# Kernel optimization log

Hardware: AMD Instinct MI355X
Metric: run time of the kernel (lower is better)

The kernel has to match this reference:

```python
import jax, jax.numpy as jnp
import numpy as np

D = 256      # d_model (module-level constant in source)
H = 4        # num_heads
HD = D // H  # head dim = 64
B = 16
T = 512
STEP = 0.5   # self.step_size
NEG = -1e9
SCALE = 1.0 / np.sqrt(HD).astype(np.float32)


def _ln(x, g, b):
    m = jnp.mean(x, -1, keepdims=True)
    v = jnp.var(x, -1, keepdims=True)
    return (x - m) / jnp.sqrt(v + 1e-5) * g + b


def _forward(x, h0,
             sa_wq, sa_wk, sa_wv, sa_wo, sa_bq, sa_bk, sa_bv, sa_bo,
             f_w1, f_b1, f_w2, f_b2,
             ta_wq, ta_wk, ta_wv, ta_wo, ta_bq, ta_bk, ta_bv, ta_bo,
             tr_w1, tr_b1, tr_w2, tr_b2,
             ps_w, ps_b, sp_w, sp_b,
             ln1_g, ln1_b, ln2_g, ln2_b, ln3_g, ln3_b, ln4_g, ln4_b):
    Bz, Tz, Dz = x.shape
    # ---- causal self-attention over parallel_repr ----
    q = (x @ sa_wq + sa_bq).reshape(Bz, Tz, H, HD)
    k = (x @ sa_wk + sa_bk).reshape(Bz, Tz, H, HD)
    v = (x @ sa_wv + sa_bv).reshape(Bz, Tz, H, HD)
    scores = jnp.einsum('bqhd,bkhd->bhqk', q, k) * SCALE
    causal = jnp.tril(jnp.ones((Tz, Tz), bool))
    scores = jnp.where(causal, scores, NEG)
    attn = jnp.einsum('bhqk,bkhd->bqhd', jax.nn.softmax(scores, -1), v)
    attn = attn.reshape(Bz, Tz, Dz) @ sa_wo + sa_bo
    x = _ln(x + attn, ln1_g, ln1_b)
    # ---- FFN with sequential guidance ----
    guid = h0 @ sp_w + sp_b                      # sequential_to_parallel, [B, D]
    ffn_in = x + 0.3 * guid[:, None, :]
    ffn = jax.nn.gelu(ffn_in @ f_w1 + f_b1, approximate=False) @ f_w2 + f_b2
    x = _ln(x + ffn, ln2_g, ln2_b)
    # ---- sequential scan with growing-cache trajectory attention ----
    # past states only enter through their K/V projections, so project each
    # new state once when it is appended (same math as re-projecting the cache).
    def step(carry, inp):
        h, kbuf, vbuf = carry                    # kbuf/vbuf: [T, B, H, HD]
        t, xt = inp                              # xt: [B, D]
        qt = (xt @ ta_wq + ta_bq).reshape(Bz, H, HD)
        sc = jnp.einsum('bhd,tbhd->bht', qt, kbuf) * SCALE
        valid = (jnp.arange(Tz) < t)[None, None, :]
        ctx = jnp.einsum('bht,tbhd->bhd',
                         jax.nn.softmax(jnp.where(valid, sc, NEG), -1), vbuf)
        ctx = ctx.reshape(Bz, Dz) @ ta_wo + ta_bo
        ctx = jnp.where(t > 0, ctx, 0.0)         # torch code zeroes context at t=0
        pg = xt @ ps_w + ps_b                    # parallel_to_sequential
        comb = jnp.concatenate([xt + 0.3 * pg, ctx], -1)
        delta = jax.nn.gelu(comb @ tr_w1 + tr_b1, approximate=False) @ tr_w2 + tr_b2
        h = _ln(h + STEP * delta, ln3_g, ln3_b)
        kbuf = kbuf.at[t].set((h @ ta_wk + ta_bk).reshape(Bz, H, HD))
        vbuf = vbuf.at[t].set((h @ ta_wv + ta_bv).reshape(Bz, H, HD))
        return (h, kbuf, vbuf), None

    buf0 = jnp.zeros((Tz, Bz, H, HD), x.dtype)
    (hT, _, _), _ = jax.lax.scan(step, (h0, buf0, buf0),
                                 (jnp.arange(Tz), jnp.swapaxes(x, 0, 1)))
    return x, _ln(hT, ln4_g, ln4_b)


def setup_inputs() -> dict:
    ks = iter(jax.random.split(jax.random.key(0), 64))
    def w(*shape):
        return jax.random.normal(next(ks), shape, jnp.float32) * 0.02
    inp = {
        'x': jax.random.normal(next(ks), (B, T, D), jnp.float32),
        'h0': jax.random.normal(next(ks), (B, D), jnp.float32),
        'sa_wq': w(D, D), 'sa_wk': w(D, D), 'sa_wv': w(D, D), 'sa_wo': w(D, D),
        'sa_bq': w(D), 'sa_bk': w(D), 'sa_bv': w(D), 'sa_bo': w(D),
        'f_w1': w(D, 4 * D), 'f_b1': w(4 * D), 'f_w2': w(4 * D, D), 'f_b2': w(D),
        'ta_wq': w(D, D), 'ta_wk': w(D, D), 'ta_wv': w(D, D), 'ta_wo': w(D, D),
        'ta_bq': w(D), 'ta_bk': w(D), 'ta_bv': w(D), 'ta_bo': w(D),
        'tr_w1': w(2 * D, 2 * D), 'tr_b1': w(2 * D), 'tr_w2': w(2 * D, D), 'tr_b2': w(D),
        'ps_w': w(D, D), 'ps_b': w(D), 'sp_w': w(D, D), 'sp_b': w(D),
        'ln1_g': jnp.ones(D), 'ln1_b': jnp.zeros(D),
        'ln2_g': jnp.ones(D), 'ln2_b': jnp.zeros(D),
        'ln3_g': jnp.ones(D), 'ln3_b': jnp.zeros(D),
        'ln4_g': jnp.ones(D), 'ln4_b': jnp.zeros(D),
    }
    return inp


def reference(x, h0,
              sa_wq, sa_wk, sa_wv, sa_wo, sa_bq, sa_bk, sa_bv, sa_bo,
              f_w1, f_b1, f_w2, f_b2,
              ta_wq, ta_wk, ta_wv, ta_wo, ta_bq, ta_bk, ta_bv, ta_bo,
              tr_w1, tr_b1, tr_w2, tr_b2,
              ps_w, ps_b, sp_w, sp_b,
              ln1_g, ln1_b, ln2_g, ln2_b, ln3_g, ln3_b, ln4_g, ln4_b):
    return _forward(x, h0,
                    sa_wq, sa_wk, sa_wv, sa_wo, sa_bq, sa_bk, sa_bv, sa_bo,
                    f_w1, f_b1, f_w2, f_b2,
                    ta_wq, ta_wk, ta_wv, ta_wo, ta_bq, ta_bk, ta_bv, ta_bo,
                    tr_w1, tr_b1, tr_w2, tr_b2,
                    ps_w, ps_b, sp_w, sp_b,
                    ln1_g, ln1_b, ln2_g, ln2_b, ln3_g, ln3_b, ln4_g, ln4_b)
```

## Files before the change

kernel.cpp:

```cpp
#include <hip/hip_runtime.h>
#include <hip/hip_bf16.h>

typedef __bf16 bf16x8 __attribute__((ext_vector_type(8)));
typedef float f32x4 __attribute__((ext_vector_type(4)));

__device__ __forceinline__ float b2f(ushort u){
  union { uint u; float f; } x; x.u = ((uint)u) << 16; return x.f;
}
__device__ __forceinline__ ushort f2b(float f){
  union { float f; uint u; } x; x.f = f;
  uint r = x.u + 0x7fff + ((x.u >> 16) & 1);
  return (ushort)(r >> 16);
}
__device__ __forceinline__ uint pack_bf2(float a, float b){
  return (uint)f2b(a) | ((uint)f2b(b) << 16);
}
__device__ __forceinline__ float lo16(uint u){ union{uint a;float f;}x; x.a=u<<16; return x.f; }
__device__ __forceinline__ float hi16(uint u){ union{uint a;float f;}x; x.a=u&0xffff0000u; return x.f; }
__device__ __forceinline__ float gelu_exact(float v){
  return 0.5f * v * (1.0f + erff(v * 0.70710678118654752f));
}

template<int AF32, int ACT>
__global__ __launch_bounds__(256) void gemm_kernel(
    const void* __restrict__ Av, const float* __restrict__ W, int ldw,
    const float* __restrict__ bias, const float* residf,
    float* Cf, ushort* Cb,
    int M, int N, int K, float scale)
{
  __shared__ __align__(16) ushort Al[64*40];
  __shared__ __align__(16) ushort Bl[64*40];
  const int nb = N >> 6;
  const int rb = blockIdx.x / nb, cb = blockIdx.x % nb;
  const int tid = threadIdx.x;
  const int w = tid >> 6, l = tid & 63;
  f32x4 acc[4];
#pragma unroll
  for(int i=0;i<4;i++) acc[i] = (f32x4){0.f,0.f,0.f,0.f};
  const int ar = tid >> 2, ai = (tid & 3) << 3;
  const int bk = tid >> 3, bn = (tid & 7) << 3;
  for(int kb = 0; kb < K; kb += 32){
    uint4 au;
    if(AF32){
      const float* Ap = (const float*)Av + (size_t)(rb*64 + ar)*K + kb + ai;
      float4 f0 = *(const float4*)Ap;
      float4 f1 = *(const float4*)(Ap + 4);
      au.x = pack_bf2(f0.x,f0.y); au.y = pack_bf2(f0.z,f0.w);
      au.z = pack_bf2(f1.x,f1.y); au.w = pack_bf2(f1.z,f1.w);
    } else {
      au = *(const uint4*)((const ushort*)Av + (size_t)(rb*64 + ar)*K + kb + ai);
    }
    const float* Wp = W + (size_t)(kb + bk)*ldw + cb*64 + bn;
    float4 w0 = *(const float4*)Wp;
    float4 w1 = *(const float4*)(Wp + 4);
    ushort bs[8];
    bs[0]=f2b(w0.x); bs[1]=f2b(w0.y); bs[2]=f2b(w0.z); bs[3]=f2b(w0.w);
    bs[4]=f2b(w1.x); bs[5]=f2b(w1.y); bs[6]=f2b(w1.z); bs[7]=f2b(w1.w);
    __syncthreads();
    *(uint4*)&Al[ar*40 + ai] = au;
#pragma unroll
    for(int i=0;i<8;i++) Bl[(bn+i)*40 + bk] = bs[i];
    __syncthreads();
    bf16x8 af = *(const bf16x8*)&Al[(w*16 + (l&15))*40 + (l>>4)*8];
#pragma unroll
    for(int c4=0;c4<4;c4++){
      bf16x8 bfv = *(const bf16x8*)&Bl[(c4*16 + (l&15))*40 + (l>>4)*8];
      acc[c4] = __builtin_amdgcn_mfma_f32_16x16x32_bf16(af, bfv, acc[c4], 0,0,0);
    }
  }
#pragma unroll
  for(int c4=0;c4<4;c4++){
#pragma unroll
    for(int r=0;r<4;r++){
      int row = rb*64 + w*16 + (l>>4)*4 + r;
      int col = cb*64 + c4*16 + (l&15);
      size_t idx = (size_t)row*N + col;
      float vv = acc[c4][r];
      if(bias) vv += bias[col];
      vv *= scale;
      if(residf) vv += residf[idx];
      if(ACT) vv = gelu_exact(vv);
      if(Cf) Cf[idx] = vv;
      if(Cb) Cb[idx] = f2b(vv);
    }
  }
}

__global__ __launch_bounds__(256) void attn_kernel(const ushort* __restrict__ Q,
    const ushort* __restrict__ K, const ushort* __restrict__ V, ushort* __restrict__ O)
{
  __shared__ float s[16*520];
  __shared__ float kt[64*66];
  __shared__ float rowm[16], rowr[16], redx[256];
  const int bid = blockIdx.x;
  const int qb = bid & 31, h = (bid>>5)&3, b = bid>>7;
  const int tid = threadIdx.x;
  const int qi = tid >> 4, jj = tid & 15;
  const int qrow = qb*16 + qi;
  float qreg[64];
  {
    const ushort* qp = Q + ((size_t)(b*512 + qrow))*256 + h*64;
#pragma unroll
    for(int d=0; d<64; d++) qreg[d] = b2f(qp[d])*0.125f;
  }
  const int ntile = (qb*16 + 79) >> 6;
  for(int jt=0; jt<ntile; jt++){
    {
      int jr = tid >> 2, d0 = (tid & 3) << 4;
      const ushort* kp = K + ((size_t)(b*512 + jt*64 + jr))*256 + h*64 + d0;
#pragma unroll
      for(int i=0;i<16;i++) kt[jr*66 + d0 + i] = b2f(kp[i]);
    }
    __syncthreads();
#pragma unroll
    for(int jl=0;jl<4;jl++){
      int jloc = jj*4 + jl;
      int j = jt*64 + jloc;
      float a = 0.f;
#pragma unroll
      for(int d=0; d<64; d++) a += qreg[d]*kt[jloc*66 + d];
      s[qi*520 + j] = (j <= qrow) ? a : -1e30f;
    }
    __syncthreads();
  }
  const int nj = ntile*64;
  float m = -1e30f;
  for(int j=jj; j<nj; j+=16) m = fmaxf(m, s[qi*520 + j]);
  redx[jj*16 + qi] = m;
  __syncthreads();
  if(tid < 16){
    float mm = -1e30f;
#pragma unroll
    for(int k2=0;k2<16;k2++) mm = fmaxf(mm, redx[k2*16 + tid]);
    rowm[tid] = mm;
  }
  __syncthreads();
  float mrow = rowm[qi];
  float ssum = 0.f;
  for(int j=jj; j<nj; j+=16){
    float e = __expf(s[qi*520+j] - mrow);
    s[qi*520+j] = e; ssum += e;
  }
  redx[jj*16 + qi] = ssum;
  __syncthreads();
  if(tid < 16){
    float t2 = 0.f;
#pragma unroll
    for(int k2=0;k2<16;k2++) t2 += redx[k2*16 + tid];
    rowr[tid] = 1.0f/t2;
  }
  const int dd = jj;
  float acc4[4] = {0,0,0,0};
  for(int jt=0; jt<ntile; jt++){
    __syncthreads();
    {
      int jr = tid >> 2, d0 = (tid & 3) << 4;
      const ushort* vp = V + ((size_t)(b*512 + jt*64 + jr))*256 + h*64 + d0;
#pragma unroll
      for(int i=0;i<16;i++) kt[jr*66 + d0 + i] = b2f(vp[i]);
    }
    __syncthreads();
#pragma unroll
    for(int jl=0;jl<64;jl++){
      float p = s[qi*520 + jt*64 + jl];
#pragma unroll
      for(int i=0;i<4;i++) acc4[i] += p*kt[jl*66 + dd*4 + i];
    }
  }
  float rr = rowr[qi];
  ushort* op = O + ((size_t)(b*512 + qrow))*256 + h*64 + dd*4;
#pragma unroll
  for(int i=0;i<4;i++) op[i] = f2b(acc4[i]*rr);
}

__global__ __launch_bounds__(256) void ln_kernel(const float* __restrict__ in,
    const float* __restrict__ g, const float* __restrict__ be,
    float* outf, ushort* outb)
{
  int row = blockIdx.x*4 + (threadIdx.x>>6);
  int lane = threadIdx.x & 63;
  size_t idx = (size_t)row*256 + lane*4;
  float4 v = *(const float4*)(in + idx);
  float s1 = v.x+v.y+v.z+v.w;
  float s2 = v.x*v.x + v.y*v.y + v.z*v.z + v.w*v.w;
#pragma unroll
  for(int off=32; off; off>>=1){ s1 += __shfl_xor(s1,off); s2 += __shfl_xor(s2,off); }
  float mu = s1*(1.f/256.f);
  float var = s2*(1.f/256.f) - mu*mu;
  float r = rsqrtf(var + 1e-5f);
  float vals[4] = {v.x,v.y,v.z,v.w};
  float4 o4; ushort4 ob;
  float* oo = (float*)&o4; ushort* obp = (ushort*)&ob;
#pragma unroll
  for(int i=0;i<4;i++){
    int d = lane*4 + i;
    float y = (vals[i]-mu)*r*g[d] + be[d];
    oo[i] = y; obp[i] = f2b(y);
  }
  if(outf) *(float4*)(outf+idx) = o4;
  if(outb) *(ushort4*)(outb+idx) = ob;
}

__global__ void guid_kernel(const float* __restrict__ h0, const float* __restrict__ spw,
                            const float* __restrict__ spb, float* __restrict__ guid)
{
  int b = blockIdx.x, c = threadIdx.x;
  float s = spb[c];
  for(int r=0;r<256;r++) s += h0[b*256+r]*spw[r*256+c];
  guid[b*256+c] = s;
}

__global__ void ffnin_kernel(const float* __restrict__ x1, const float* __restrict__ guid,
                             ushort* __restrict__ out)
{
  size_t base = ((size_t)blockIdx.x*256 + threadIdx.x)*8;
  int row = (int)(base >> 8); int bb = row >> 9; int c = (int)(base & 255);
  float4 v0 = *(const float4*)(x1 + base);
  float4 v1 = *(const float4*)(x1 + base + 4);
  const float* gp = guid + bb*256 + c;
  const float* xs = (const float*)&v0;
  ushort o[8];
#pragma unroll
  for(int i=0;i<4;i++) o[i] = f2b(xs[i] + 0.3f*gp[i]);
  const float* xs1 = (const float*)&v1;
#pragma unroll
  for(int i=0;i<4;i++) o[4+i] = f2b(xs1[i] + 0.3f*gp[4+i]);
  *(uint4*)(out + base) = *(uint4*)o;
}

__global__ void bo_kernel(const float* __restrict__ ta_bo, const float* __restrict__ tr_w1,
                          float* __restrict__ bo_f)
{
  int c = threadIdx.x;
  float s = 0.f;
  for(int m=0;m<256;m++) s += ta_bo[m]*tr_w1[(size_t)(256+m)*512 + c];
  bo_f[c] = s;
}

__global__ __launch_bounds__(512, 1) void scan_kernel(
    const ushort* __restrict__ qtb, const ushort* __restrict__ Ubf,
    const float* __restrict__ Wf, const float* __restrict__ bo_f,
    float* cbuf, float* dbuf, int* flags,
    const float* __restrict__ ta_wk, const float* __restrict__ ta_wv,
    const float* __restrict__ ta_bk, const float* __restrict__ ta_bv,
    const float* __restrict__ tr_w2, const float* __restrict__ tr_b2,
    const float* __restrict__ ln3_g, const float* __restrict__ ln3_b,
    const float* __restrict__ ln4_g, const float* __restrict__ ln4_b,
    const float* __restrict__ h0, float* __restrict__ out_h)
{
  __shared__ __align__(16) float red[2][1024];
  __shared__ float pbuf[512];
  __shared__ __align__(16) float hbuf[256];
  __shared__ float ctxL[256];
  __shared__ float qbufS[2][64];
  __shared__ float mG[2][16], sG[2][16];
  __shared__ float sLastP[4];
  __shared__ float glbuf[128];
  __shared__ int cp_same[4];
  extern __shared__ __align__(16) ushort dynL[];
  ushort* kcL = dynL;
  ushort* vcL = dynL + 512*66;

  const int tid = threadIdx.x;
  const int bid = blockIdx.x;
  const int b = bid & 15;
  const int role = bid >> 4;

  if(role < 4){
    for(int i = tid; i < 512*66; i += 512){ kcL[i] = 0; vcL[i] = 0; }
  }

  int myxcc;
  asm volatile("s_getreg_b32 %0, hwreg(HW_REG_XCC_ID)" : "=s"(myxcc));
  if(tid == 0)
    __hip_atomic_store(&flags[256 + bid], myxcc + 1, __ATOMIC_RELEASE, __HIP_MEMORY_SCOPE_AGENT);
  if(tid < 4){
    int cbid = (role < 4) ? (64 + tid*16 + b) : (tid*16 + b);
    int v;
    while((v = __hip_atomic_load(&flags[256 + cbid], __ATOMIC_ACQUIRE, __HIP_MEMORY_SCOPE_AGENT)) == 0)
      __builtin_amdgcn_s_sleep(8);
    cp_same[tid] = ((v - 1) == myxcc);
  }
  __syncthreads();
  const int anyrem = !(cp_same[0] && cp_same[1] && cp_same[2] && cp_same[3]);

  if(role < 4){
    const int hd = role;
    const int bh = b*4 + hd;
    const int out = tid >> 2, sX = tid & 3;
    const int kvSel = out >> 6, colX = out & 63;
    const float* WX = kvSel ? ta_wv : ta_wk;
    uint wp[32];
#pragma unroll
    for(int i=0;i<32;i++){
      int r0 = 8*i + 2*sX;
      wp[i] = pack_bf2(WX[(size_t)r0*256 + hd*64 + colX],
                       WX[(size_t)(r0+1)*256 + hd*64 + colX]);
    }
    const float pbX = kvSel ? ta_bv[hd*64 + colX] : ta_bk[hd*64 + colX];
    float h4[4], b2r4[4], g34[4], b34[4];
    if(tid < 64){
#pragma unroll
      for(int c=0;c<4;c++){
        int d = 4*tid + c;
        h4[c] = h0[b*256 + d]; b2r4[c] = tr_b2[d]; g34[c] = ln3_g[d]; b34[c] = ln3_b[d];
      }
      *(float4*)&hbuf[4*tid] = *(float4*)h4;
    }
    const int j_sh = (tid >= 64) ? (tid - 64) : (448 + tid);
    const int gsh = j_sh >> 5;
    const int lsh = tid & 31;
    __syncthreads();

    ushort qpre = 0;
    if(tid >= 448) qpre = qtb[((size_t)(b*512 + 1))*256 + hd*64 + (tid - 448)];

#pragma clang loop unroll(disable)
    for(int t=0;t<512;t++){
      if(tid >= 448){
        qbufS[(t+1)&1][tid-448] = b2f(qpre)*0.125f;
        int tq = (t+2 < 512) ? (t+2) : 511;
        qpre = qtb[((size_t)(b*512 + tq))*256 + hd*64 + (tid - 448)];
      }
      if(t > 0){
        float acc = 0.f;
#pragma unroll
        for(int i=0;i<32;i++){
          int r0 = 8*i + 2*sX;
          acc += hbuf[r0]*lo16(wp[i]) + hbuf[r0+1]*hi16(wp[i]);
        }
        acc += __shfl_xor(acc, 1);
        acc += __shfl_xor(acc, 2);
        float kf = acc + pbX;
        if(sX == 0){
          ushort u = f2b(kf);
          if(kvSel == 0) kcL[(t-1)*66 + colX] = u;
          else           vcL[(t-1)*66 + colX] = u;
        }
        float pv = (kvSel == 0 && sX == 0) ? qbufS[t&1][colX]*kf : 0.f;
        pv += __shfl_xor(pv, 4);
        pv += __shfl_xor(pv, 8);
        pv += __shfl_xor(pv, 16);
        pv += __shfl_xor(pv, 32);
        if(tid < 256 && (tid & 63) == 0) sLastP[tid >> 6] = pv;
        __syncthreads();
        if(tid < 64){
          const int par = t & 1;
          float sl = (sLastP[0] + sLastP[1]) + (sLastP[2] + sLastP[3]);
          float m = sl;
#pragma unroll
          for(int g=0; g<16; g++) m = fmaxf(m, mG[par][g]);
          float el = __expf(sl - m);
          float Z = el;
          float num = el * b2f(vcL[(t-1)*66 + tid]);
#pragma unroll
          for(int g=0; g<16; g++){
            float scl = __expf(mG[par][g] - m);
            Z   += sG[par][g]*scl;
            num += red[par][g*64 + tid]*scl;
          }
          cbuf[b*256 + hd*64 + tid] = num / Z;
          asm volatile("s_waitcnt vmcnt(0)" ::: "memory");
          if(tid == 0){
            *(volatile int*)&flags[bh] = t;
            if(anyrem)
              __hip_atomic_store(&flags[128 + bh], t, __ATOMIC_RELEASE, __HIP_MEMORY_SCOPE_AGENT);
          }
        }
      }

      {
        const int par = (t+1)&1;
        float s = -3.0e38f;
        if(j_sh < t){
          const uint* kr = (const uint*)(kcL + j_sh*66);
          const float* qS = qbufS[par];
          float a = 0.f;
#pragma unroll
          for(int w=0; w<32; w++){
            uint kk = kr[w];
            a += qS[2*w]*lo16(kk) + qS[2*w+1]*hi16(kk);
          }
          s = a;
        }
        float gm = s;
#pragma unroll
        for(int off=16; off; off>>=1) gm = fmaxf(gm, __shfl_xor(gm, off));
        float e = (j_sh < t) ? __expf(s - gm) : 0.f;
        pbuf[j_sh] = e;
        float gs = e;
#pragma unroll
        for(int off=16; off; off>>=1) gs += __shfl_xor(gs, off);
        if(lsh == 0){ mG[par][gsh] = gm; sG[par][gsh] = gs; }
        int nn = t - gsh*32; nn = nn < 0 ? 0 : (nn > 32 ? 32 : nn);
        float a0 = 0.f, a1 = 0.f;
        const uint* vbase = (const uint*)vcL;
#pragma unroll 4
        for(int i=0;i<nn;i++){
          int j2 = gsh*32 + i;
          uint vv = vbase[j2*33 + lsh];
          float p = pbuf[j2];
          a0 += p*lo16(vv); a1 += p*hi16(vv);
        }
        float2 pr; pr.x = a0; pr.y = a1;
        *(float2*)&red[par][gsh*64 + 2*lsh] = pr;
      }

      if(tid < 4){
        if(cp_same[tid]){
          while(*(volatile int*)&flags[64 + b*4 + tid] < t+1) __builtin_amdgcn_s_sleep(1);
        } else {
          while(__hip_atomic_load(&flags[192 + b*4 + tid], __ATOMIC_RELAXED, __HIP_MEMORY_SCOPE_AGENT) < t+1)
            __builtin_amdgcn_s_sleep(2);
        }
      }
      if(tid < 64){
        if(anyrem) __builtin_amdgcn_fence(__ATOMIC_ACQUIRE, "agent");
        float ds[4] = {0.f,0.f,0.f,0.f};
#pragma unroll
        for(int i=0;i<4;i++){
#pragma unroll
          for(int c=0;c<4;c++)
            ds[c] += *(volatile float*)&dbuf[(b*4+i)*256 + 4*tid + c];
        }
        float v4[4]; float s1 = 0.f, s2 = 0.f;
#pragma unroll
        for(int c=0;c<4;c++){
          v4[c] = h4[c] + 0.5f*(ds[c] + b2r4[c]);
          s1 += v4[c]; s2 += v4[c]*v4[c];
        }
#pragma unroll
        for(int off=32; off; off>>=1){ s1 += __shfl_xor(s1,off); s2 += __shfl_xor(s2,off); }
        float mu = s1*(1.f/256.f);
        float qq = s2*(1.f/256.f) - mu*mu;
        float rstd = rsqrtf(qq + 1e-5f);
#pragma unroll
        for(int c=0;c<4;c++) h4[c] = (v4[c]-mu)*rstd*g34[c] + b34[c];
        *(float4*)&hbuf[4*tid] = *(float4*)h4;
      }
      __syncthreads();
    }

    if(hd == 0 && tid < 64){
      float s1 = 0.f, s2 = 0.f;
#pragma unroll
      for(int c=0;c<4;c++){ s1 += h4[c]; s2 += h4[c]*h4[c]; }
#pragma unroll
      for(int off=32; off; off>>=1){ s1 += __shfl_xor(s1,off); s2 += __shfl_xor(s2,off); }
      float mu = s1*(1.f/256.f);
      float qq = s2*(1.f/256.f) - mu*mu;
      float rstd = rsqrtf(qq + 1e-5f);
#pragma unroll
      for(int c=0;c<4;c++){
        int d = 4*tid + c;
        out_h[b*256 + d] = (h4[c]-mu)*rstd*ln4_g[d] + ln4_b[d];
      }
    }
  } else {
    const int ish = role - 4;
    const int hid = tid >> 2, sY = tid & 3;
    const int colY = ish*128 + hid;
    uint wfp[32];
#pragma unroll
    for(int i=0;i<32;i++){
      int r0 = 8*i + 2*sY;
      wfp[i] = pack_bf2(Wf[(size_t)r0*512 + colY], Wf[(size_t)(r0+1)*512 + colY]);
    }
    const int dcol = tid >> 1, s2 = tid & 1;
    uint w2p[32];
#pragma unroll
    for(int i=0;i<32;i++){
      int r0 = ish*128 + 4*i + 2*s2;
      w2p[i] = pack_bf2(tr_w2[(size_t)r0*256 + dcol], tr_w2[(size_t)(r0+1)*256 + dcol]);
    }
    const float borr = (sY==0) ? bo_f[colY] : 0.f;
    __syncthreads();

#pragma clang loop unroll(disable)
    for(int t=0;t<512;t++){
      ushort uvs = 0;
      if(sY == 0) uvs = Ubf[((size_t)(b*512 + t))*512 + colY];
      if(t > 0){
        if(tid < 256){
          int q = tid >> 6;
          if(cp_same[q]){
            while(*(volatile int*)&flags[b*4 + q] < t) __builtin_amdgcn_s_sleep(1);
          } else {
            while(__hip_atomic_load(&flags[128 + b*4 + q], __ATOMIC_RELAXED, __HIP_MEMORY_SCOPE_AGENT) < t)
              __builtin_amdgcn_s_sleep(2);
          }
        }
        if(anyrem) __builtin_amdgcn_fence(__ATOMIC_ACQUIRE, "agent");
        if(tid < 256) ctxL[tid] = *(volatile float*)&cbuf[b*256 + tid];
      }
      __syncthreads();
      float accf = 0.f;
      if(t > 0){
#pragma unroll
        for(int i=0;i<32;i++){
          int r0 = 8*i + 2*sY;
          accf += ctxL[r0]*lo16(wfp[i]) + ctxL[r0+1]*hi16(wfp[i]);
        }
        accf += __shfl_xor(accf, 1);
        accf += __shfl_xor(accf, 2);
      }
      if(sY == 0){
        float g1 = b2f(uvs) + ((t>0) ? (borr + accf) : 0.f);
        glbuf[hid] = gelu_exact(g1);
      }
      __syncthreads();
      {
        float dp = 0.f;
#pragma unroll
        for(int i=0;i<32;i++){
          int r0 = 4*i + 2*s2;
          dp += glbuf[r0]*lo16(w2p[i]) + glbuf[r0+1]*hi16(w2p[i]);
        }
        dp += __shfl_xor(dp, 1);
        if(s2 == 0) dbuf[(b*4+ish)*256 + dcol] = dp;
      }
      asm volatile("s_waitcnt vmcnt(0)" ::: "memory");
      __syncthreads();
      if(tid == 0){
        *(volatile int*)&flags[64 + b*4 + ish] = t+1;
        if(anyrem)
          __hip_atomic_store(&flags[192 + b*4 + ish], t+1, __ATOMIC_RELEASE, __HIP_MEMORY_SCOPE_AGENT);
      }
    }
  }
}

#define OFF_FLAGS ((size_t)0)
#define OFF_BOF   ((size_t)2048)
#define OFF_CBUF  ((size_t)4096)
#define OFF_DBUF  ((size_t)20480)
#define OFF_GUID  ((size_t)86016)
#define OFF_WF    ((size_t)131072)
#define OFF_Z1    ((size_t)(1u<<20))
#define OFF_Z2    ((size_t)(5u<<20))
#define OFF_Z3    ((size_t)(9u<<20))
#define OFF_Z4    ((size_t)(13u<<20))
#define OFF_M     ((size_t)(17u<<20))

#define SCAN_DYN_LDS (512*66*2*2)

extern "C" void kernel_launch(void* const* d_in, const int* in_sizes, int n_in,
                              void* d_out, int out_size, void* d_ws, size_t ws_size,
                              hipStream_t stream)
{
  const float* x     = (const float*)d_in[0];
  const float* h0    = (const float*)d_in[1];
  const float* sa_wq = (const float*)d_in[2];
  const float* sa_wk = (const float*)d_in[3];
  const float* sa_wv = (const float*)d_in[4];
  const float* sa_wo = (const float*)d_in[5];
  const float* sa_bq = (const float*)d_in[6];
  const float* sa_bk = (const float*)d_in[7];
  const float* sa_bv = (const float*)d_in[8];
  const float* sa_bo = (const float*)d_in[9];
  const float* f_w1  = (const float*)d_in[10];
  const float* f_b1  = (const float*)d_in[11];
  const float* f_w2  = (const float*)d_in[12];
  const float* f_b2  = (const float*)d_in[13];
  const float* ta_wq = (const float*)d_in[14];
  const float* ta_wk = (const float*)d_in[15];
  const float* ta_wv = (const float*)d_in[16];
  const float* ta_wo = (const float*)d_in[17];
  const float* ta_bq = (const float*)d_in[18];
  const float* ta_bk = (const float*)d_in[19];
  const float* ta_bv = (const float*)d_in[20];
  const float* ta_bo = (const float*)d_in[21];
  const float* tr_w1 = (const float*)d_in[22];
  const float* tr_b1 = (const float*)d_in[23];
  const float* tr_w2 = (const float*)d_in[24];
  const float* tr_b2 = (const float*)d_in[25];
  const float* ps_w  = (const float*)d_in[26];
  const float* ps_b  = (const float*)d_in[27];
  const float* sp_w  = (const float*)d_in[28];
  const float* sp_b  = (const float*)d_in[29];
  const float* ln1_g = (const float*)d_in[30];
  const float* ln1_b = (const float*)d_in[31];
  const float* ln2_g = (const float*)d_in[32];
  const float* ln2_b = (const float*)d_in[33];
  const float* ln3_g = (const float*)d_in[34];
  const float* ln3_b = (const float*)d_in[35];
  const float* ln4_g = (const float*)d_in[36];
  const float* ln4_b = (const float*)d_in[37];

  char* ws = (char*)d_ws;
  int*    flags = (int*)   (ws + OFF_FLAGS);
  float*  bo_f  = (float*) (ws + OFF_BOF);
  float*  cbuf  = (float*) (ws + OFF_CBUF);
  float*  dbuf  = (float*) (ws + OFF_DBUF);
  float*  guid  = (float*) (ws + OFF_GUID);
  float*  Wff   = (float*) (ws + OFF_WF);
  ushort* qb    = (ushort*)(ws + OFF_Z1);
  ushort* kb    = (ushort*)(ws + OFF_Z2);
  ushort* vb    = (ushort*)(ws + OFF_Z3);
  ushort* attnb = (ushort*)(ws + OFF_Z4);
  float*  x0pre = (float*) (ws + OFF_Z1);
  float*  x1f   = (float*) (ws + OFF_Z3);
  ushort* ffnb  = (ushort*)(ws + OFF_M);
  ushort* mid   = (ushort*)(ws + OFF_M + (4u<<20));
  float*  x2pre = (float*) (ws + OFF_Z1);
  ushort* abf   = (ushort*)(ws + OFF_Z4);
  ushort* qtb   = (ushort*)(ws + OFF_Z3);
  ushort* Ubf   = (ushort*)(ws + OFF_M);
  float*  outb  = (float*)d_out;
  float*  out_h = outb + (out_size - 4096);

  static int attr_done = 0;
  if(!attr_done){
    hipFuncSetAttribute((const void*)scan_kernel,
                        hipFuncAttributeMaxDynamicSharedMemorySize, SCAN_DYN_LDS);
    attr_done = 1;
  }

  hipMemsetAsync(flags, 0, 2048, stream);

  gemm_kernel<1,0><<<512, 256, 0, stream>>>(x, sa_wq, 256, sa_bq, nullptr, nullptr, qb, 8192,256,256, 1.0f);
  gemm_kernel<1,0><<<512, 256, 0, stream>>>(x, sa_wk, 256, sa_bk, nullptr, nullptr, kb, 8192,256,256, 1.0f);
  gemm_kernel<1,0><<<512, 256, 0, stream>>>(x, sa_wv, 256, sa_bv, nullptr, nullptr, vb, 8192,256,256, 1.0f);
  attn_kernel<<<2048, 256, 0, stream>>>(qb, kb, vb, attnb);
  gemm_kernel<0,0><<<512, 256, 0, stream>>>(attnb, sa_wo, 256, sa_bo, x, x0pre, nullptr, 8192,256,256, 1.0f);
  ln_kernel<<<2048, 256, 0, stream>>>(x0pre, ln1_g, ln1_b, x1f, nullptr);
  guid_kernel<<<16, 256, 0, stream>>>(h0, sp_w, sp_b, guid);
  ffnin_kernel<<<1024, 256, 0, stream>>>(x1f, guid, ffnb);
  gemm_kernel<0,1><<<1024, 256, 0, stream>>>(ffnb, f_w1, 1024, f_b1, nullptr, nullptr, mid, 8192,512,256, 1.0f);
  gemm_kernel<0,0><<<512, 256, 0, stream>>>(mid, f_w2, 256, f_b2, x1f, x2pre, nullptr, 8192,256,512, 1.0f);
  gemm_kernel<0,1><<<1024, 256, 0, stream>>>(ffnb, f_w1 + 512, 1024, f_b1 + 512, nullptr, nullptr, mid, 8192,512,256, 1.0f);
  gemm_kernel<0,0><<<512, 256, 0, stream>>>(mid, f_w2 + (size_t)512*256, 256, nullptr, x2pre, x2pre, nullptr, 8192,256,512, 1.0f);
  ln_kernel<<<2048, 256, 0, stream>>>(x2pre, ln2_g, ln2_b, outb, nullptr);

  gemm_kernel<1,0><<<512, 256, 0, stream>>>(outb, ps_w, 256, ps_b, outb, nullptr, abf, 8192,256,256, 0.3f);
  gemm_kernel<0,0><<<1024, 256, 0, stream>>>(abf, tr_w1, 512, tr_b1, nullptr, nullptr, Ubf, 8192,512,256, 1.0f);
  gemm_kernel<1,0><<<512, 256, 0, stream>>>(outb, ta_wq, 256, ta_bq, nullptr, nullptr, qtb, 8192,256,256, 1.0f);
  gemm_kernel<1,0><<<32, 256, 0, stream>>>(ta_wo, tr_w1 + (size_t)256*512, 512, nullptr, nullptr, Wff, nullptr, 256,512,256, 1.0f);
  bo_kernel<<<1, 512, 0, stream>>>(ta_bo, tr_w1, bo_f);

  scan_kernel<<<128, 512, SCAN_DYN_LDS, stream>>>(qtb, Ubf, Wff, bo_f, cbuf, dbuf, flags,
                                                  ta_wk, ta_wv, ta_bk, ta_bv, tr_w2, tr_b2,
                                                  ln3_g, ln3_b, ln4_g, ln4_b, h0, out_h);
}
```

Measured before the change: 4.266 ms.

## Precombine softmax partials off the critical path and use per-wave ready flags

Moves the 16-group softmax merge (max, rescaled Z and numerator) into the previous iteration, right after the partial products are written. The critical-path step then only folds in the newest key. The producer blocks drop their block-wide barrier before signalling and instead publish one ready flag per wave, which the consumer polls with 32 threads. LDS reads become float2 vector loads. This adds a __syncthreads in the attention role and enlarges the flag region and workspace offsets.

```diff
diff --git a/kernel.cpp b/kernel.cpp
--- a/kernel.cpp
+++ b/kernel.cpp
@@ -249,13 +249,15 @@
     const float* __restrict__ h0, float* __restrict__ out_h)
 {
   __shared__ __align__(16) float red[2][1024];
-  __shared__ float pbuf[512];
+  __shared__ __align__(16) float pbuf[512];
   __shared__ __align__(16) float hbuf[256];
-  __shared__ float ctxL[256];
-  __shared__ float qbufS[2][64];
+  __shared__ __align__(16) float ctxL[256];
+  __shared__ __align__(16) float qbufS[2][64];
   __shared__ float mG[2][16], sG[2][16];
+  __shared__ __align__(16) float numS[2][64];
+  __shared__ float mzS[2][2];
   __shared__ float sLastP[4];
-  __shared__ float glbuf[128];
+  __shared__ __align__(16) float glbuf[128];
   __shared__ int cp_same[4];
   extern __shared__ __align__(16) ushort dynL[];
   ushort* kcL = dynL;
@@ -265,6 +267,8 @@
   const int bid = blockIdx.x;
   const int b = bid & 15;
   const int role = bid >> 4;
+  const int b4 = b*4;
+  const int w8 = tid >> 6;
 
   if(role < 4){
     for(int i = tid; i < 512*66; i += 512){ kcL[i] = 0; vcL[i] = 0; }
@@ -286,7 +290,7 @@
 
   if(role < 4){
     const int hd = role;
-    const int bh = b*4 + hd;
+    const int bh = b4 + hd;
     const int out = tid >> 2, sX = tid & 3;
     const int kvSel = out >> 6, colX = out & 63;
     const float* WX = kvSel ? ta_wv : ta_wk;
@@ -326,8 +330,8 @@
         float acc = 0.f;
 #pragma unroll
         for(int i=0;i<32;i++){
-          int r0 = 8*i + 2*sX;
-          acc += hbuf[r0]*lo16(wp[i]) + hbuf[r0+1]*hi16(wp[i]);
+          float2 hv = *(const float2*)&hbuf[8*i + 2*sX];
+          acc += hv.x*lo16(wp[i]) + hv.y*hi16(wp[i]);
         }
         acc += __shfl_xor(acc, 1);
         acc += __shfl_xor(acc, 2);
@@ -347,19 +351,13 @@
         if(tid < 64){
           const int par = t & 1;
           float sl = (sLastP[0] + sLastP[1]) + (sLastP[2] + sLastP[3]);
-          float m = sl;
-#pragma unroll
-          for(int g=0; g<16; g++) m = fmaxf(m, mG[par][g]);
+          float mo = mzS[par][0], Zo = mzS[par][1];
+          float m = fmaxf(mo, sl);
+          float so = __expf(mo - m);
           float el = __expf(sl - m);
-          float Z = el;
-          float num = el * b2f(vcL[(t-1)*66 + tid]);
-#pragma unroll
-          for(int g=0; g<16; g++){
-            float scl = __expf(mG[par][g] - m);
-            Z   += sG[par][g]*scl;
-            num += red[par][g*64 + tid]*scl;
-          }
-          cbuf[b*256 + hd*64 + tid] = num / Z;
+          float Z = Zo*so + el;
+          float vlast = b2f(vcL[(t-1)*66 + tid]);
+          cbuf[b*256 + hd*64 + tid] = (numS[par][tid]*so + el*vlast) / Z;
           asm volatile("s_waitcnt vmcnt(0)" ::: "memory");
           if(tid == 0){
             *(volatile int*)&flags[bh] = t;
@@ -379,7 +377,8 @@
 #pragma unroll
           for(int w=0; w<32; w++){
             uint kk = kr[w];
-            a += qS[2*w]*lo16(kk) + qS[2*w+1]*hi16(kk);
+            float2 q2 = *(const float2*)&qS[2*w];
+            a += q2.x*lo16(kk) + q2.y*hi16(kk);
           }
           s = a;
         }
@@ -405,12 +404,28 @@
         float2 pr; pr.x = a0; pr.y = a1;
         *(float2*)&red[par][gsh*64 + 2*lsh] = pr;
       }
-
-      if(tid < 4){
-        if(cp_same[tid]){
-          while(*(volatile int*)&flags[64 + b*4 + tid] < t+1) __builtin_amdgcn_s_sleep(1);
+      __syncthreads();
+      if(tid < 64){
+        const int par = (t+1)&1;
+        float mo = mG[par][0];
+#pragma unroll
+        for(int g=1; g<16; g++) mo = fmaxf(mo, mG[par][g]);
+        float Zo = 0.f, nm = 0.f;
+#pragma unroll
+        for(int g=0; g<16; g++){
+          float scl = __expf(mG[par][g] - mo);
+          Zo += sG[par][g]*scl;
+          nm += red[par][g*64 + tid]*scl;
+        }
+        numS[par][tid] = nm;
+        if(tid == 0){ mzS[par][0] = mo; mzS[par][1] = Zo; }
+      }
+      if(tid < 32){
+        const int sh = tid >> 3, wv = tid & 7;
+        if(cp_same[sh]){
+          while(*(volatile int*)&flags[512 + (b4+sh)*8 + wv] < t+1) __builtin_amdgcn_s_sleep(1);
         } else {
-          while(__hip_atomic_load(&flags[192 + b*4 + tid], __ATOMIC_RELAXED, __HIP_MEMORY_SCOPE_AGENT) < t+1)
+          while(__hip_atomic_load(&flags[1024 + (b4+sh)*8 + wv], __ATOMIC_RELAXED, __HIP_MEMORY_SCOPE_AGENT) < t+1)
             __builtin_amdgcn_s_sleep(2);
         }
       }
@@ -419,9 +434,10 @@
         float ds[4] = {0.f,0.f,0.f,0.f};
 #pragma unroll
         for(int i=0;i<4;i++){
+          const float* dp = &dbuf[(b4+i)*256 + 4*tid];
 #pragma unroll
           for(int c=0;c<4;c++)
-            ds[c] += *(volatile float*)&dbuf[(b*4+i)*256 + 4*tid + c];
+            ds[c] += __hip_atomic_load(dp + c, __ATOMIC_RELAXED, __HIP_MEMORY_SCOPE_AGENT);
         }
         float v4[4]; float s1 = 0.f, s2 = 0.f;
 #pragma unroll
@@ -484,9 +500,9 @@
         if(tid < 256){
           int q = tid >> 6;
           if(cp_same[q]){
-            while(*(volatile int*)&flags[b*4 + q] < t) __builtin_amdgcn_s_sleep(1);
+            while(*(volatile int*)&flags[b4 + q] < t) __builtin_amdgcn_s_sleep(1);
           } else {
-            while(__hip_atomic_load(&flags[128 + b*4 + q], __ATOMIC_RELAXED, __HIP_MEMORY_SCOPE_AGENT) < t)
+            while(__hip_atomic_load(&flags[128 + b4 + q], __ATOMIC_RELAXED, __HIP_MEMORY_SCOPE_AGENT) < t)
               __builtin_amdgcn_s_sleep(2);
           }
         }
@@ -498,8 +514,8 @@
       if(t > 0){
 #pragma unroll
         for(int i=0;i<32;i++){
-          int r0 = 8*i + 2*sY;
-          accf += ctxL[r0]*lo16(wfp[i]) + ctxL[r0+1]*hi16(wfp[i]);
+          float2 c2 = *(const float2*)&ctxL[8*i + 2*sY];
+          accf += c2.x*lo16(wfp[i]) + c2.y*hi16(wfp[i]);
         }
         accf += __shfl_xor(accf, 1);
         accf += __shfl_xor(accf, 2);
@@ -513,28 +529,27 @@
         float dp = 0.f;
 #pragma unroll
         for(int i=0;i<32;i++){
-          int r0 = 4*i + 2*s2;
-          dp += glbuf[r0]*lo16(w2p[i]) + glbuf[r0+1]*hi16(w2p[i]);
+          float2 gv = *(const float2*)&glbuf[4*i + 2*s2];
+          dp += gv.x*lo16(w2p[i]) + gv.y*hi16(w2p[i]);
         }
         dp += __shfl_xor(dp, 1);
-        if(s2 == 0) dbuf[(b*4+ish)*256 + dcol] = dp;
+        if(s2 == 0) dbuf[(b4+ish)*256 + dcol] = dp;
       }
       asm volatile("s_waitcnt vmcnt(0)" ::: "memory");
-      __syncthreads();
-      if(tid == 0){
-        *(volatile int*)&flags[64 + b*4 + ish] = t+1;
+      if((tid & 63) == 0){
+        *(volatile int*)&flags[512 + (b4+ish)*8 + w8] = t+1;
         if(anyrem)
-          __hip_atomic_store(&flags[192 + b*4 + ish], t+1, __ATOMIC_RELEASE, __HIP_MEMORY_SCOPE_AGENT);
+          __hip_atomic_store(&flags[1024 + (b4+ish)*8 + w8], t+1, __ATOMIC_RELEASE, __HIP_MEMORY_SCOPE_AGENT);
       }
     }
   }
 }
 
 #define OFF_FLAGS ((size_t)0)
-#define OFF_BOF   ((size_t)2048)
-#define OFF_CBUF  ((size_t)4096)
-#define OFF_DBUF  ((size_t)20480)
-#define OFF_GUID  ((size_t)86016)
+#define OFF_BOF   ((size_t)8192)
+#define OFF_CBUF  ((size_t)16384)
+#define OFF_DBUF  ((size_t)32768)
+#define OFF_GUID  ((size_t)98304)
 #define OFF_WF    ((size_t)131072)
 #define OFF_Z1    ((size_t)(1u<<20))
 #define OFF_Z2    ((size_t)(5u<<20))
@@ -616,7 +631,7 @@
     attr_done = 1;
   }
 
-  hipMemsetAsync(flags, 0, 2048, stream);
+  hipMemsetAsync(flags, 0, 8192, stream);
 
   gemm_kernel<1,0><<<512, 256, 0, stream>>>(x, sa_wq, 256, sa_bq, nullptr, nullptr, qb, 8192,256,256, 1.0f);
   gemm_kernel<1,0><<<512, 256, 0, stream>>>(x, sa_wk, 256, sa_bk, nullptr, nullptr, kb, 8192,256,256, 1.0f);
```

Result: faster. 3.526 ms (-17.4%).
